# Kernel tuning notes

Hardware: AMD Instinct MI355X
Metric: run time of the kernel (lower is better)

## Reference

```python
import jax, jax.numpy as jnp
import numpy as np

# omega = exp(i*pi/4), omega^8 = 1. Basis elements of ExactScalar are omega^p for
# p in (0, 1, 2, 7) (UNIT_PHASES row 3 = [0,0,0,-1] => omega^3 = -e3 => e3 = omega^7).
_UNIT_PHASES = np.array([
    [1, 0, 0, 0], [0, 1, 0, 0], [0, 0, 1, 0], [0, 0, 0, -1],
    [-1, 0, 0, 0], [0, -1, 0, 0], [0, 0, -1, 0], [0, 0, 0, 1],
], dtype=np.int32)
_BASIS_EXP = np.array([0, 1, 2, 7])
# Structure tensor of the ring: e_i * e_j = omega^(p_i + p_j) expressed in the basis.
_MUL = _UNIT_PHASES[(_BASIS_EXP[:, None] + _BASIS_EXP[None, :]) % 8]  # (4, 4, 4)
_IDENTITY = np.array([1, 0, 0, 0], dtype=np.int32)


def setup_inputs() -> dict:
    B, G, T, P = 256, 2048, 16, 64  # batch, num_graphs, max_terms, n_params
    key = jax.random.key(0)
    k1, k2, k3, k4 = jax.random.split(key, 4)
    phases = jax.random.randint(k1, (G, T), 0, 8, dtype=jnp.int32)
    params = jax.random.randint(k2, (G, T, P), 0, 2, dtype=jnp.int32)
    counts = jax.random.randint(k3, (G,), 1, T + 1, dtype=jnp.int32)
    param_vals = jax.random.randint(k4, (B, P), 0, 2, dtype=jnp.int32)
    # 1 + omega^k lookup table (float storage; cast to int32 inside reference).
    one_plus_phases = jnp.asarray(_UNIT_PHASES, jnp.float32).at[:, 0].add(1.0)
    return dict(phases=phases, params=params, counts=counts,
                param_vals=param_vals, one_plus_phases=one_plus_phases)


def reference(phases, params, counts, param_vals, one_plus_phases):
    # GF(2) matmul: parity of selected params per (batch, graph, term).
    rowsum = jnp.einsum('gtp,bp->bgt', params, param_vals) % 2  # (B, G, T)
    phase_idx = (4 * rowsum + phases[None, :, :]) % 8           # (B, G, T)
    table = one_plus_phases.astype(jnp.int32)                   # (8, 4)
    term_vals = table[phase_idx]                                # (B, G, T, 4)
    # Mask padded slots to the multiplicative identity.
    T = phases.shape[1]
    mask = jnp.arange(T)[None, :] < counts[:, None]             # (G, T)
    ident = jnp.asarray(_IDENTITY)
    term_vals = jnp.where(mask[None, :, :, None], term_vals, ident)
    # Associative product over terms in the ExactScalar ring (tree reduction).
    mul_tab = jnp.asarray(_MUL)                                 # (4, 4, 4)
    x = term_vals
    while x.shape[2] > 1:
        if x.shape[2] % 2:  # pad odd length with identity
            pad = jnp.broadcast_to(ident, x.shape[:2] + (1, 4))
            x = jnp.concatenate([x, pad], axis=2)
        x = jnp.einsum('bgti,bgtj,ijk->bgtk', x[:, :, 0::2, :], x[:, :, 1::2, :], mul_tab)
    return x[:, :, 0, :]  # (B, G, 4) ExactScalar coefficients
```

## Files before the change

kernel.cpp:

```cpp
#include <hip/hip_runtime.h>
#include <hip/hip_bf16.h>

#define NP_B 256
#define NP_G 2048
#define NP_T 16
#define NP_P 64
#define NP_NB 2

__global__ __launch_bounds__(256) void np_pack_kernel(
    const int* __restrict__ params,
    const int* __restrict__ param_vals,
    const int* __restrict__ phases,
    unsigned long long* __restrict__ ppT,
    unsigned long long* __restrict__ pvp,
    unsigned long long* __restrict__ phw)
{
    const int wid  = (blockIdx.x * blockDim.x + threadIdx.x) >> 6;
    const int lane = threadIdx.x & 63;

    if (wid < NP_G * NP_T) {
        const int gt = wid;
        const int v  = params[gt * NP_P + lane];
        const unsigned long long m = __ballot(v != 0);
        if (lane == 0) {
            const int g = gt >> 4;
            const int t = gt & 15;
            ppT[t * NP_G + g] = m;
        }
    } else if (wid < NP_G * NP_T + NP_B) {
        const int b = wid - NP_G * NP_T;
        const int v = param_vals[b * NP_P + lane];
        const unsigned long long m = __ballot(v != 0);
        if (lane == 0) pvp[b] = m;
    } else {
        const int g = (wid - (NP_G * NP_T + NP_B)) * 64 + lane;
        if (g < NP_G) {
            unsigned long long w = 0ull;
            #pragma unroll
            for (int t = 0; t < NP_T; ++t)
                w |= (unsigned long long)(phases[g * NP_T + t] & 7) << (4 * t);
            phw[g] = w;
        }
    }
}

__global__ __launch_bounds__(256) void np_main_kernel(
    const unsigned long long* __restrict__ ppT,
    const unsigned long long* __restrict__ pvp,
    const unsigned long long* __restrict__ phw,
    const int* __restrict__ counts,
    int* __restrict__ out)
{
    const int g  = blockIdx.x * 256 + threadIdx.x;
    const int b0 = blockIdx.y * NP_NB;

    unsigned long long pm[NP_T];
    #pragma unroll
    for (int t = 0; t < NP_T; ++t) pm[t] = ppT[t * NP_G + g];

    unsigned long long pv[NP_NB];
    #pragma unroll
    for (int i = 0; i < NP_NB; ++i) pv[i] = pvp[b0 + i];

    const unsigned long long ph = phw[g];
    const int count = counts[g];

    int c[NP_NB][4];
    #pragma unroll
    for (int i = 0; i < NP_NB; ++i) {
        c[i][0] = 1; c[i][1] = 0; c[i][2] = 0; c[i][3] = 0;
    }

    #pragma unroll
    for (int t = 0; t < NP_T; ++t) {
        const int p  = (int)((ph >> (4 * t)) & 7);
        const bool r1 = (p & 1) != 0;
        const bool r2 = (p & 2) != 0;
        const int  s0 = (p >> 2) & 1;

        if (t < count) {
            #pragma unroll
            for (int i = 0; i < NP_NB; ++i) {
                const int parity = (int)(__popcll(pm[t] & pv[i]) & 1);
                const int sign   = s0 ^ parity;
                const int m      = -sign;

                const int x0 = r1 ? -c[i][3] : c[i][0];
                const int x1 = r1 ?  c[i][0] : c[i][1];
                const int x2 = r1 ?  c[i][1] : c[i][2];
                const int x3 = r1 ?  c[i][2] : c[i][3];
                const int y0 = r2 ? -x2 : x0;
                const int y1 = r2 ? -x3 : x1;
                const int y2 = r2 ?  x0 : x2;
                const int y3 = r2 ?  x1 : x3;

                c[i][0] += (y0 ^ m) + sign;
                c[i][1] += (y1 ^ m) + sign;
                c[i][2] += (y2 ^ m) + sign;
                c[i][3] += (y3 ^ m) + sign;
            }
        }
    }

    #pragma unroll
    for (int i = 0; i < NP_NB; ++i) {
        int4 r;
        r.x = c[i][0]; r.y = c[i][1]; r.z = c[i][2]; r.w = -c[i][3];
        ((int4*)out)[(b0 + i) * NP_G + g] = r;
    }
}

extern "C" void kernel_launch(void* const* d_in, const int* in_sizes, int n_in,
                              void* d_out, int out_size, void* d_ws, size_t ws_size,
                              hipStream_t stream) {
    const int* phases     = (const int*)d_in[0];
    const int* params     = (const int*)d_in[1];
    const int* counts     = (const int*)d_in[2];
    const int* param_vals = (const int*)d_in[3];

    int* out = (int*)d_out;

    unsigned long long* ppT = (unsigned long long*)d_ws;
    unsigned long long* pvp = ppT + NP_G * NP_T;
    unsigned long long* phw = pvp + NP_B;

    const int waves = NP_G * NP_T + NP_B + (NP_G + 63) / 64;
    const int pack_blocks = (waves * 64 + 255) / 256;
    np_pack_kernel<<<pack_blocks, 256, 0, stream>>>(
        params, param_vals, phases, ppT, pvp, phw);

    dim3 grid(NP_G / 256, NP_B / NP_NB);
    np_main_kernel<<<grid, 256, 0, stream>>>(ppT, pvp, phw, counts, out);
}
```

Baseline: 80.69 us.

## Fuse bit-packing and ring-product kernels into one shared-memory kernel

Merges the separate pack kernel and main kernel into a single launch. Each 512-thread block ballots the params rows for 4 graphs into shared memory and packs all batch param masks into shared memory, then computes the products. This removes the workspace round trip and one launch. In exchange, the batch masks are repacked in every block, and output stores become 64-byte strided chunks instead of fully contiguous wave writes.

```diff
diff --git a/kernel.cpp b/kernel.cpp
--- a/kernel.cpp
+++ b/kernel.cpp
@@ -1,87 +1,87 @@
 #include <hip/hip_runtime.h>
-#include <hip/hip_bf16.h>
 
 #define NP_B 256
 #define NP_G 2048
 #define NP_T 16
 #define NP_P 64
-#define NP_NB 2
 
-__global__ __launch_bounds__(256) void np_pack_kernel(
+__global__ __launch_bounds__(512) void np_fused_kernel(
     const int* __restrict__ params,
     const int* __restrict__ param_vals,
     const int* __restrict__ phases,
-    unsigned long long* __restrict__ ppT,
-    unsigned long long* __restrict__ pvp,
-    unsigned long long* __restrict__ phw)
-{
-    const int wid  = (blockIdx.x * blockDim.x + threadIdx.x) >> 6;
-    const int lane = threadIdx.x & 63;
-
-    if (wid < NP_G * NP_T) {
-        const int gt = wid;
-        const int v  = params[gt * NP_P + lane];
-        const unsigned long long m = __ballot(v != 0);
-        if (lane == 0) {
-            const int g = gt >> 4;
-            const int t = gt & 15;
-            ppT[t * NP_G + g] = m;
-        }
-    } else if (wid < NP_G * NP_T + NP_B) {
-        const int b = wid - NP_G * NP_T;
-        const int v = param_vals[b * NP_P + lane];
-        const unsigned long long m = __ballot(v != 0);
-        if (lane == 0) pvp[b] = m;
-    } else {
-        const int g = (wid - (NP_G * NP_T + NP_B)) * 64 + lane;
-        if (g < NP_G) {
-            unsigned long long w = 0ull;
-            #pragma unroll
-            for (int t = 0; t < NP_T; ++t)
-                w |= (unsigned long long)(phases[g * NP_T + t] & 7) << (4 * t);
-            phw[g] = w;
-        }
-    }
-}
-
-__global__ __launch_bounds__(256) void np_main_kernel(
-    const unsigned long long* __restrict__ ppT,
-    const unsigned long long* __restrict__ pvp,
-    const unsigned long long* __restrict__ phw,
     const int* __restrict__ counts,
     int* __restrict__ out)
 {
-    const int g  = blockIdx.x * 256 + threadIdx.x;
-    const int b0 = blockIdx.y * NP_NB;
+    __shared__ unsigned long long s_pm[4][17];
+    __shared__ unsigned long long s_pv[NP_B];
 
-    unsigned long long pm[NP_T];
+    const int tid  = threadIdx.x;
+    const int wid  = tid >> 6;
+    const int lane = tid & 63;
+    const int g0   = blockIdx.x * 4;
+
     #pragma unroll
-    for (int t = 0; t < NP_T; ++t) pm[t] = ppT[t * NP_G + g];
+    for (int k = 0; k < 8; ++k) {
+        const int r = wid * 8 + k;
+        const int v = params[(g0 * NP_T + r) * NP_P + lane];
+        const unsigned long long m = __ballot(v != 0);
+        if (lane == 0) s_pm[r >> 4][r & 15] = m;
+    }
 
-    unsigned long long pv[NP_NB];
+    if (tid < NP_B) {
+        const int4* pv4 = (const int4*)(param_vals + tid * NP_P);
+        unsigned long long m = 0ull;
+        #pragma unroll
+        for (int k = 0; k < 16; ++k) {
+            const int4 v = pv4[k];
+            const unsigned long long nib =
+                (unsigned long long)((v.x & 1) | ((v.y & 1) << 1) |
+                                     ((v.z & 1) << 2) | ((v.w & 1) << 3));
+            m |= nib << (4 * k);
+        }
+        s_pv[tid] = m;
+    }
+
+    const int g_l = tid & 3;
+    const int g   = g0 + g_l;
+    const int b0  = (tid >> 2) * 2;
+
+    const int4* ph4 = (const int4*)(phases + g * NP_T);
+    unsigned long long ph = 0ull;
     #pragma unroll
-    for (int i = 0; i < NP_NB; ++i) pv[i] = pvp[b0 + i];
-
-    const unsigned long long ph = phw[g];
+    for (int k = 0; k < 4; ++k) {
+        const int4 v = ph4[k];
+        ph |= (unsigned long long)(v.x & 7) << (16 * k);
+        ph |= (unsigned long long)(v.y & 7) << (16 * k + 4);
+        ph |= (unsigned long long)(v.z & 7) << (16 * k + 8);
+        ph |= (unsigned long long)(v.w & 7) << (16 * k + 12);
+    }
     const int count = counts[g];
 
-    int c[NP_NB][4];
+    __syncthreads();
+
+    const unsigned long long pv0 = s_pv[b0];
+    const unsigned long long pv1 = s_pv[b0 + 1];
+
+    int c[2][4];
     #pragma unroll
-    for (int i = 0; i < NP_NB; ++i) {
+    for (int i = 0; i < 2; ++i) {
         c[i][0] = 1; c[i][1] = 0; c[i][2] = 0; c[i][3] = 0;
     }
 
     #pragma unroll
     for (int t = 0; t < NP_T; ++t) {
-        const int p  = (int)((ph >> (4 * t)) & 7);
+        const int p   = (int)((ph >> (4 * t)) & 7);
         const bool r1 = (p & 1) != 0;
         const bool r2 = (p & 2) != 0;
         const int  s0 = (p >> 2) & 1;
 
         if (t < count) {
+            const unsigned long long pm = s_pm[g_l][t];
             #pragma unroll
-            for (int i = 0; i < NP_NB; ++i) {
-                const int parity = (int)(__popcll(pm[t] & pv[i]) & 1);
+            for (int i = 0; i < 2; ++i) {
+                const unsigned long long pv = i ? pv1 : pv0;
+                const int parity = (int)(__popcll(pm & pv) & 1);
                 const int sign   = s0 ^ parity;
                 const int m      = -sign;
 
@@ -103,7 +103,7 @@
     }
 
     #pragma unroll
-    for (int i = 0; i < NP_NB; ++i) {
+    for (int i = 0; i < 2; ++i) {
         int4 r;
         r.x = c[i][0]; r.y = c[i][1]; r.z = c[i][2]; r.w = -c[i][3];
         ((int4*)out)[(b0 + i) * NP_G + g] = r;
@@ -120,15 +120,5 @@
 
     int* out = (int*)d_out;
 
-    unsigned long long* ppT = (unsigned long long*)d_ws;
-    unsigned long long* pvp = ppT + NP_G * NP_T;
-    unsigned long long* phw = pvp + NP_B;
-
-    const int waves = NP_G * NP_T + NP_B + (NP_G + 63) / 64;
-    const int pack_blocks = (waves * 64 + 255) / 256;
-    np_pack_kernel<<<pack_blocks, 256, 0, stream>>>(
-        params, param_vals, phases, ppT, pvp, phw);
-
-    dim3 grid(NP_G / 256, NP_B / NP_NB);
-    np_main_kernel<<<grid, 256, 0, stream>>>(ppT, pvp, phw, counts, out);
+    np_fused_kernel<<<512, 512, 0, stream>>>(params, param_vals, phases, counts, out);
 }
```

After: 81.96 us. About the same (+1.6%).
